# Kernel tuning notes

Hardware: AMD Instinct MI355X
Metric: run time of the kernel (lower is better)

The kernel has to match this reference:

```python
import jax, jax.numpy as jnp
import numpy as np
from jax import lax

R, BS, NATM, NORB = 2, 128, 81, 240
M_DIM = 16


def _init(key, shape, scale=0.05):
    return (jax.random.normal(key, shape) * scale).astype(jnp.float32)


def setup_inputs() -> dict:
    key = jax.random.key(0)
    ks = jax.random.split(key, 24)
    return {
        "xyz": jax.random.normal(ks[0], (R, BS, NATM, 3), jnp.float32) * 3.0,
        "cn": jax.random.uniform(ks[1], (R, BS, NATM), jnp.float32),
        "edisp": jax.random.normal(ks[2], (R, BS, NATM), jnp.float32),
        "ovlp": jax.random.normal(ks[3], (R, BS, NORB, NORB), jnp.float32),
        "h0": jax.random.normal(ks[4], (R, BS, NORB, NORB), jnp.float32),
        "egfn1": jax.random.normal(ks[5], (R, BS), jnp.float32),
        "nu": jax.random.normal(ks[6], (BS, R), jnp.float32),
        # EGNN(dim=2): edge_input_dim = 2*dim + 1 = 5
        "We1": _init(ks[7], (10, 5)), "be1": jnp.zeros((10,), jnp.float32),
        "We2": _init(ks[8], (M_DIM, 10)), "be2": jnp.zeros((M_DIM,), jnp.float32),
        "Wc1": _init(ks[9], (M_DIM * 4, M_DIM)), "bc1": jnp.zeros((M_DIM * 4,), jnp.float32),
        "Wc2": _init(ks[10], (1, M_DIM * 4)), "bc2": jnp.zeros((1,), jnp.float32),
        "coors_scale": jnp.full((1,), 1e-2, jnp.float32),
        "Wn1": _init(ks[11], (4, 2 + M_DIM)), "bn1": jnp.zeros((4,), jnp.float32),
        "Wn2": _init(ks[12], (2, 4)), "bn2": jnp.zeros((2,), jnp.float32),
        "conv1_w": _init(ks[13], (2, 1, 2, 2), 0.2), "conv1_b": jnp.zeros((2,), jnp.float32),
        "conv2_w": _init(ks[14], (2, 2, 2, 2), 0.2), "conv2_b": jnp.zeros((2,), jnp.float32),
        "fc1_w": _init(ks[15], (60, 14087), 0.01), "fc1_b": jnp.zeros((60,), jnp.float32),
        "fc2_w": _init(ks[16], (30, 60)), "fc2_b": jnp.zeros((30,), jnp.float32),
        "fc3_w": _init(ks[17], (1, 30)), "fc3_b": jnp.zeros((1,), jnp.float32),
    }


def _egnn(feats, coors, We1, be1, We2, be2, Wc1, bc1, Wc2, bc2, scale, Wn1, bn1, Wn2, bn2):
    # feats: (b, n, 2), coors: (b, n, 3); dense all-pairs EGNN layer (lucidrains defaults)
    b, n, d = feats.shape
    rel = coors[:, :, None, :] - coors[:, None, :, :]            # (b, i, j, 3)
    rel_dist = jnp.sum(rel * rel, axis=-1, keepdims=True)        # (b, i, j, 1) squared dist
    fi = jnp.broadcast_to(feats[:, :, None, :], (b, n, n, d))
    fj = jnp.broadcast_to(feats[:, None, :, :], (b, n, n, d))
    edge_in = jnp.concatenate([fi, fj, rel_dist], axis=-1)       # (b, i, j, 5)
    m = jax.nn.silu(edge_in @ We1.T + be1)
    m = jax.nn.silu(m @ We2.T + be2)                             # (b, i, j, M_DIM)
    cw = (jax.nn.silu(m @ Wc1.T + bc1) @ Wc2.T + bc2)[..., 0]    # (b, i, j)
    # CoorsNorm: unit-normalize rel coords, learned scale (init 1e-2)
    norm = jnp.sqrt(jnp.clip(rel_dist, 1e-16, None))
    rel_n = rel / norm * scale
    coors_out = jnp.einsum('bij,bijc->bic', cw, rel_n) + coors
    m_i = jnp.sum(m, axis=2)                                     # sum pooling over j
    node_in = jnp.concatenate([feats, m_i], axis=-1)
    feats_out = jax.nn.silu(node_in @ Wn1.T + bn1) @ Wn2.T + bn2 + feats
    return feats_out, coors_out


def _maxpool2(x):
    return lax.reduce_window(x, -jnp.inf, lax.max, (1, 1, 2, 2), (1, 1, 2, 2), 'VALID')


def _conv_block(x, w1, b1, w2, b2):
    # x: (b, N, N) -> NCHW conv stack matching conv1/pool/conv2/pool
    x = x[:, None, :, :]
    x = lax.conv_general_dilated(x, w1, (1, 1), 'VALID', dimension_numbers=('NCHW', 'OIHW', 'NCHW'))
    x = _maxpool2(jax.nn.leaky_relu(x + b1[None, :, None, None]))
    x = lax.conv_general_dilated(x, w2, (1, 1), 'VALID', dimension_numbers=('NCHW', 'OIHW', 'NCHW'))
    x = _maxpool2(jax.nn.leaky_relu(x + b2[None, :, None, None]))
    return x


def reference(xyz, cn, edisp, ovlp, h0, egfn1, nu,
              We1, be1, We2, be2, Wc1, bc1, Wc2, bc2, coors_scale,
              Wn1, bn1, Wn2, bn2, conv1_w, conv1_b, conv2_w, conv2_b,
              fc1_w, fc1_b, fc2_w, fc2_b, fc3_w, fc3_b):
    contribs = []
    for i in range(R):  # fixed small reactant list, mirrors the Python loop
        feats = jnp.stack([cn[i], edisp[i]], axis=-1)            # (bs, n_atms, 2)
        atm, _ = _egnn(feats, xyz[i], We1, be1, We2, be2, Wc1, bc1, Wc2, bc2,
                       coors_scale, Wn1, bn1, Wn2, bn2)
        o = _conv_block(ovlp[i], conv1_w, conv1_b, conv2_w, conv2_b)
        h = _conv_block(h0[i], conv1_w, conv1_b, conv2_w, conv2_b)
        x = jnp.concatenate([o, h], axis=1).reshape(o.shape[0], -1)   # (bs, 4*59*59)
        x = jnp.concatenate([x, atm.reshape(atm.shape[0], -1), egfn1[i][:, None]], axis=1)
        x = jax.nn.leaky_relu(x @ fc1_w.T + fc1_b)
        x = jax.nn.leaky_relu(x @ fc2_w.T + fc2_b)
        x = x @ fc3_w.T + fc3_b                                   # (bs, 1)
        contribs.append(x * nu[:, i][:, None])
    return jnp.sum(jnp.concatenate(contribs, axis=1), axis=1)    # (bs,)
```

## Files before the change

### kernel.cpp

```cpp
#include <hip/hip_runtime.h>
#include <hip/hip_bf16.h>

#define XDIM 14087
#define NATM 81
#define BS   128
#define KC   128
#define NKCH 111

__device__ __forceinline__ float fast_rcp(float x) {
    return __builtin_amdgcn_rcpf(x);
}
__device__ __forceinline__ float silu(float z) {
    return z * fast_rcp(1.f + __expf(-z));
}
__device__ __forceinline__ float leaky(float z) {
    return (z > 0.f) ? z : 0.01f * z;
}

__global__ __launch_bounds__(512) void egnn_kernel(
    const float* __restrict__ xyz, const float* __restrict__ cn,
    const float* __restrict__ edisp, const float* __restrict__ egfn1,
    const float* __restrict__ We1, const float* __restrict__ be1,
    const float* __restrict__ We2, const float* __restrict__ be2,
    const float* __restrict__ Wn1, const float* __restrict__ bn1,
    const float* __restrict__ Wn2, const float* __restrict__ bn2,
    float* __restrict__ xbuf)
{
    const int bid = blockIdx.x;
    const int tid = threadIdx.x;

    __shared__ float sc[NATM][3];
    __shared__ float sf[NATM][2];
    __shared__ float sai[NATM][10];
    __shared__ float sbj[NATM][10];
    __shared__ float sW2[160];
    __shared__ float sbe2[16];
    __shared__ float sw5[10];
    __shared__ float sWn1[72];
    __shared__ float sbn1[4];
    __shared__ float sWn2[8];
    __shared__ float sbn2[2];
    __shared__ float smp[3][NATM][17];

    const float* xb = xyz + (size_t)bid * NATM * 3;
    for (int idx = tid; idx < NATM * 3; idx += 512) sc[idx / 3][idx % 3] = xb[idx];
    if (tid < NATM) {
        const float f0 = cn[(size_t)bid * NATM + tid];
        const float f1 = edisp[(size_t)bid * NATM + tid];
        sf[tid][0] = f0; sf[tid][1] = f1;
        #pragma unroll
        for (int k = 0; k < 10; ++k) {
            sai[tid][k] = be1[k] + We1[k * 5 + 0] * f0 + We1[k * 5 + 1] * f1;
            sbj[tid][k] =          We1[k * 5 + 2] * f0 + We1[k * 5 + 3] * f1;
        }
    }
    if (tid < 160) sW2[tid] = We2[tid];
    if (tid < 16)  sbe2[tid] = be2[tid];
    if (tid < 10)  sw5[tid] = We1[tid * 5 + 4];
    if (tid < 72)  sWn1[tid] = Wn1[tid];
    if (tid < 4)   sbn1[tid] = bn1[tid];
    if (tid < 8)   sWn2[tid] = Wn2[tid];
    if (tid < 2)   sbn2[tid] = bn2[tid];
    __syncthreads();

    if (tid < 486) {
        const int i    = tid % 81;
        const int part = (tid / 81) % 3;
        const int half = tid / 243;

        float W2r[80];
        #pragma unroll
        for (int q = 0; q < 80; ++q) W2r[q] = sW2[half * 80 + q];
        float be2r[8];
        #pragma unroll
        for (int q = 0; q < 8; ++q) be2r[q] = sbe2[half * 8 + q];
        float w5r[10];
        #pragma unroll
        for (int k = 0; k < 10; ++k) w5r[k] = sw5[k];
        float air[10];
        #pragma unroll
        for (int k = 0; k < 10; ++k) air[k] = sai[i][k];
        const float ci0 = sc[i][0], ci1 = sc[i][1], ci2 = sc[i][2];

        float macc[8];
        #pragma unroll
        for (int q = 0; q < 8; ++q) macc[q] = 0.f;

        const int j0 = part * 27;
        for (int j = j0; j < j0 + 27; ++j) {
            const float dx = ci0 - sc[j][0];
            const float dy = ci1 - sc[j][1];
            const float dz = ci2 - sc[j][2];
            const float rd = dx * dx + dy * dy + dz * dz;
            float h[10];
            #pragma unroll
            for (int k = 0; k < 10; ++k) {
                const float z = air[k] + sbj[j][k] + w5r[k] * rd;
                h[k] = silu(z);
            }
            #pragma unroll
            for (int q = 0; q < 8; ++q) {
                float z = be2r[q];
                #pragma unroll
                for (int k = 0; k < 10; ++k) z += W2r[q * 10 + k] * h[k];
                macc[q] += silu(z);
            }
        }
        #pragma unroll
        for (int q = 0; q < 8; ++q) smp[part][i][half * 8 + q] = macc[q];
    }
    __syncthreads();

    if (tid < NATM) {
        float mi[16];
        #pragma unroll
        for (int q = 0; q < 16; ++q)
            mi[q] = smp[0][tid][q] + smp[1][tid][q] + smp[2][tid][q];
        const float f0 = sf[tid][0], f1 = sf[tid][1];
        float n1[4];
        #pragma unroll
        for (int k = 0; k < 4; ++k) {
            float z = sbn1[k] + sWn1[k * 18 + 0] * f0 + sWn1[k * 18 + 1] * f1;
            #pragma unroll
            for (int q = 0; q < 16; ++q) z += sWn1[k * 18 + 2 + q] * mi[q];
            n1[k] = silu(z);
        }
        float* xrow = xbuf + (size_t)bid * XDIM + 13924 + tid * 2;
        #pragma unroll
        for (int c = 0; c < 2; ++c) {
            float z = sbn2[c] + (c ? f1 : f0);
            #pragma unroll
            for (int k = 0; k < 4; ++k) z += sWn2[c * 4 + k] * n1[k];
            xrow[c] = z;
        }
    }
    if (tid == 0) xbuf[(size_t)bid * XDIM + 14086] = egfn1[bid];
}

__global__ __launch_bounds__(256) void conv_kernel(
    const float* __restrict__ ovlp, const float* __restrict__ h0,
    const float* __restrict__ w1, const float* __restrict__ b1,
    const float* __restrict__ w2, const float* __restrict__ b2,
    float* __restrict__ xbuf)
{
    const int bid   = blockIdx.x;
    const int strip = bid % 15;
    const int img   = bid / 15;
    const int b     = img & 127;
    const int t     = (img >> 7) & 1;
    const int r     = img >> 8;
    const int tid   = threadIdx.x;

    const int wv = tid >> 6;
    const int l  = tid & 63;
    const int y  = strip * 4 + wv;
    const int x  = l;
    if (x >= 59 || y >= 59) return;

    const float4* src4 = reinterpret_cast<const float4*>(
        (t ? h0 : ovlp) + (size_t)(r * BS + b) * 57600);

    float w1r[8], w2r[16], b1r[2], b2r[2];
    #pragma unroll
    for (int k = 0; k < 8; ++k) w1r[k] = w1[k];
    #pragma unroll
    for (int k = 0; k < 16; ++k) w2r[k] = w2[k];
    b1r[0] = b1[0]; b1r[1] = b1[1];
    b2r[0] = b2[0]; b2r[1] = b2[1];

    float P[7][8];
    const int base = 4 * y * 60 + x;
    #pragma unroll
    for (int rr = 0; rr < 7; ++rr) {
        const float4 a  = src4[base + rr * 60];
        const float4 bq = src4[base + rr * 60 + 1];
        P[rr][0] = a.x;  P[rr][1] = a.y;  P[rr][2] = a.z;  P[rr][3] = a.w;
        P[rr][4] = bq.x; P[rr][5] = bq.y; P[rr][6] = bq.z; P[rr][7] = bq.w;
    }

    float p1[2][3][3];
    #pragma unroll
    for (int c = 0; c < 2; ++c) {
        const float wa = w1r[c * 4 + 0], wb = w1r[c * 4 + 1];
        const float wc = w1r[c * 4 + 2], wd = w1r[c * 4 + 3];
        const float bb = b1r[c];
        #pragma unroll
        for (int pp = 0; pp < 3; ++pp)
        #pragma unroll
        for (int qq = 0; qq < 3; ++qq) {
            float mx = -3.4e38f;
            #pragma unroll
            for (int s = 0; s < 2; ++s)
            #pragma unroll
            for (int tt = 0; tt < 2; ++tt) {
                const int u = 2 * pp + s, v = 2 * qq + tt;
                float a = fmaf(wa, P[u][v], fmaf(wb, P[u][v + 1],
                          fmaf(wc, P[u + 1][v], fmaf(wd, P[u + 1][v + 1], bb))));
                a = leaky(a);
                mx = fmaxf(mx, a);
            }
            p1[c][pp][qq] = mx;
        }
    }

    float* xrow = xbuf + (size_t)(r * BS + b) * XDIM + (size_t)(t * 2) * 3481
                  + y * 59 + x;
    #pragma unroll
    for (int c2 = 0; c2 < 2; ++c2) {
        float mx = -3.4e38f;
        #pragma unroll
        for (int a2 = 0; a2 < 2; ++a2)
        #pragma unroll
        for (int b2i = 0; b2i < 2; ++b2i) {
            float acc = b2r[c2];
            #pragma unroll
            for (int c1 = 0; c1 < 2; ++c1)
            #pragma unroll
            for (int du = 0; du < 2; ++du)
            #pragma unroll
            for (int dv = 0; dv < 2; ++dv)
                acc += w2r[((c2 * 2 + c1) * 2 + du) * 2 + dv]
                     * p1[c1][a2 + du][b2i + dv];
            mx = fmaxf(mx, leaky(acc));
        }
        xrow[(size_t)c2 * 3481] = mx;
    }
}

__global__ __launch_bounds__(256) void gemm_fc1_kernel(
    const float* __restrict__ xbuf, const float* __restrict__ fc1w,
    float* __restrict__ psum)
{
    const int kc   = blockIdx.x;
    const int mt   = blockIdx.y;
    const int tid  = threadIdx.x;
    const int kbase = kc * KC;
    const int rem   = min(KC, XDIM - kbase);
    const int row0  = mt * 32;

    __shared__ float4 X4[32][33];
    __shared__ float4 W4[64][33];

    float* Xs = reinterpret_cast<float*>(&X4[0][0]);
    float* Ws = reinterpret_cast<float*>(&W4[0][0]);

    for (int idx = tid; idx < 32 * KC; idx += 256) {
        const int m = idx >> 7, k = idx & 127;
        Xs[m * 132 + k] = (k < rem) ? xbuf[(size_t)(row0 + m) * XDIM + kbase + k] : 0.f;
    }
    for (int idx = tid; idx < 64 * KC; idx += 256) {
        const int n = idx >> 7, k = idx & 127;
        Ws[n * 132 + k] = (n < 60 && k < rem) ? fc1w[(size_t)n * XDIM + kbase + k] : 0.f;
    }
    __syncthreads();

    const int ty = tid >> 4, tx = tid & 15;
    const int m0 = ty * 2;

    float acc[2][4];
    #pragma unroll
    for (int i = 0; i < 2; ++i)
    #pragma unroll
    for (int j = 0; j < 4; ++j) acc[i][j] = 0.f;

    #pragma unroll 4
    for (int k4 = 0; k4 < 32; ++k4) {
        const float4 xa = X4[m0][k4];
        const float4 xb = X4[m0 + 1][k4];
        #pragma unroll
        for (int j = 0; j < 4; ++j) {
            const float4 w = W4[tx + 16 * j][k4];
            acc[0][j] += xa.x * w.x + xa.y * w.y + xa.z * w.z + xa.w * w.w;
            acc[1][j] += xb.x * w.x + xb.y * w.y + xb.z * w.z + xb.w * w.w;
        }
    }

    float* po = psum + ((size_t)kc * 256 + row0) * 64;
    #pragma unroll
    for (int i = 0; i < 2; ++i)
    #pragma unroll
    for (int j = 0; j < 4; ++j)
        po[(size_t)(m0 + i) * 64 + tx + 16 * j] = acc[i][j];
}

__global__ __launch_bounds__(128) void fc_tail_kernel(
    const float* __restrict__ psum,
    const float* __restrict__ fc1b,
    const float* __restrict__ fc2w, const float* __restrict__ fc2b,
    const float* __restrict__ fc3w, const float* __restrict__ fc3b,
    const float* __restrict__ nu, float* __restrict__ out)
{
    const int b = blockIdx.x;
    const int tid = threadIdx.x;
    const int rh = tid >> 6;
    const int n  = tid & 63;

    __shared__ float y1s[2][64];
    __shared__ float y2s[2][30];

    const int row = rh * 128 + b;
    float s = 0.f;
    #pragma unroll 8
    for (int kcc = 0; kcc < NKCH; ++kcc)
        s += psum[((size_t)kcc * 256 + row) * 64 + n];
    y1s[rh][n] = (n < 60) ? leaky(s + fc1b[n]) : 0.f;
    __syncthreads();

    if (n < 30) {
        float a2 = fc2b[n];
        const float* wr = fc2w + n * 60;
        #pragma unroll
        for (int k = 0; k < 60; ++k) a2 += wr[k] * y1s[rh][k];
        y2s[rh][n] = leaky(a2);
    }
    __syncthreads();

    if (tid == 0) {
        float acc_out = 0.f;
        #pragma unroll
        for (int r = 0; r < 2; ++r) {
            float a3 = fc3b[0];
            #pragma unroll
            for (int k = 0; k < 30; ++k) a3 += fc3w[k] * y2s[r][k];
            acc_out += a3 * nu[b * 2 + r];
        }
        out[b] = acc_out;
    }
}

extern "C" void kernel_launch(void* const* d_in, const int* in_sizes, int n_in,
                              void* d_out, int out_size, void* d_ws, size_t ws_size,
                              hipStream_t stream)
{
    const float* xyz   = (const float*)d_in[0];
    const float* cn    = (const float*)d_in[1];
    const float* edisp = (const float*)d_in[2];
    const float* ovlp  = (const float*)d_in[3];
    const float* h0    = (const float*)d_in[4];
    const float* egfn1 = (const float*)d_in[5];
    const float* nu    = (const float*)d_in[6];
    const float* We1   = (const float*)d_in[7];
    const float* be1   = (const float*)d_in[8];
    const float* We2   = (const float*)d_in[9];
    const float* be2   = (const float*)d_in[10];
    const float* Wn1   = (const float*)d_in[16];
    const float* bn1   = (const float*)d_in[17];
    const float* Wn2   = (const float*)d_in[18];
    const float* bn2   = (const float*)d_in[19];
    const float* c1w   = (const float*)d_in[20];
    const float* c1b   = (const float*)d_in[21];
    const float* c2w   = (const float*)d_in[22];
    const float* c2b   = (const float*)d_in[23];
    const float* fc1w  = (const float*)d_in[24];
    const float* fc1b  = (const float*)d_in[25];
    const float* fc2w  = (const float*)d_in[26];
    const float* fc2b  = (const float*)d_in[27];
    const float* fc3w  = (const float*)d_in[28];
    const float* fc3b  = (const float*)d_in[29];

    float* xbuf = (float*)d_ws;
    float* psum = (float*)((char*)d_ws + 14425088);
    float* out  = (float*)d_out;

    hipLaunchKernelGGL(egnn_kernel, dim3(256), dim3(512), 0, stream,
                       xyz, cn, edisp, egfn1, We1, be1, We2, be2,
                       Wn1, bn1, Wn2, bn2, xbuf);
    hipLaunchKernelGGL(conv_kernel, dim3(2 * 2 * BS * 15), dim3(256), 0, stream,
                       ovlp, h0, c1w, c1b, c2w, c2b, xbuf);
    hipLaunchKernelGGL(gemm_fc1_kernel, dim3(NKCH, 8), dim3(256), 0, stream,
                       xbuf, fc1w, psum);
    hipLaunchKernelGGL(fc_tail_kernel, dim3(128), dim3(128), 0, stream,
                       psum, fc1b, fc2w, fc2b, fc3w, fc3b, nu, out);
}
```

Before: 274.6 us.

## Compute two conv outputs per thread to share overlapping input loads

Each conv thread now produces two adjacent output columns, loading a 7x12 input window instead of 7x8, so the overlapping pool windows are read and computed once for both outputs. The grid becomes 8 strips of 8 rows per image instead of 15 strips of 4, with clamped indices and guarded stores replacing the early return. Leaky ReLU is moved after the max (valid because it is monotonic), which cuts activation work. In exchange, more registers are used per thread and the padded lanes do redundant work.

Measured after the change: 284.8 us. 3.7% more time.

```diff
diff --git a/kernel.cpp b/kernel.cpp
--- a/kernel.cpp
+++ b/kernel.cpp
@@ -144,18 +144,18 @@
     float* __restrict__ xbuf)
 {
     const int bid   = blockIdx.x;
-    const int strip = bid % 15;
-    const int img   = bid / 15;
+    const int strip = bid & 7;
+    const int img   = bid >> 3;
     const int b     = img & 127;
     const int t     = (img >> 7) & 1;
     const int r     = img >> 8;
     const int tid   = threadIdx.x;
 
-    const int wv = tid >> 6;
-    const int l  = tid & 63;
-    const int y  = strip * 4 + wv;
-    const int x  = l;
-    if (x >= 59 || y >= 59) return;
+    const int q    = tid & 31;
+    const int slot = tid >> 5;
+    const int y    = strip * 8 + slot;
+    const int qc   = (q < 30) ? q : 29;
+    const int yc   = (y < 59) ? y : 58;
 
     const float4* src4 = reinterpret_cast<const float4*>(
         (t ? h0 : ovlp) + (size_t)(r * BS + b) * 57600);
@@ -168,62 +168,70 @@
     b1r[0] = b1[0]; b1r[1] = b1[1];
     b2r[0] = b2[0]; b2r[1] = b2[1];
 
-    float P[7][8];
-    const int base = 4 * y * 60 + x;
+    float P[7][12];
+    const int rbase = 4 * yc * 60 + 2 * qc;
     #pragma unroll
     for (int rr = 0; rr < 7; ++rr) {
-        const float4 a  = src4[base + rr * 60];
-        const float4 bq = src4[base + rr * 60 + 1];
-        P[rr][0] = a.x;  P[rr][1] = a.y;  P[rr][2] = a.z;  P[rr][3] = a.w;
-        P[rr][4] = bq.x; P[rr][5] = bq.y; P[rr][6] = bq.z; P[rr][7] = bq.w;
-    }
-
-    float p1[2][3][3];
+        #pragma unroll
+        for (int c4 = 0; c4 < 3; ++c4) {
+            const int ci = 2 * qc + c4;
+            const float4 v = src4[4 * yc * 60 + rr * 60 + ((ci < 60) ? ci : 59)];
+            P[rr][c4 * 4 + 0] = v.x; P[rr][c4 * 4 + 1] = v.y;
+            P[rr][c4 * 4 + 2] = v.z; P[rr][c4 * 4 + 3] = v.w;
+        }
+    }
+
+    float p1[2][3][5];
     #pragma unroll
     for (int c = 0; c < 2; ++c) {
         const float wa = w1r[c * 4 + 0], wb = w1r[c * 4 + 1];
         const float wc = w1r[c * 4 + 2], wd = w1r[c * 4 + 3];
         const float bb = b1r[c];
         #pragma unroll
-        for (int pp = 0; pp < 3; ++pp)
-        #pragma unroll
-        for (int qq = 0; qq < 3; ++qq) {
+        for (int pr = 0; pr < 3; ++pr)
+        #pragma unroll
+        for (int pc = 0; pc < 5; ++pc) {
             float mx = -3.4e38f;
             #pragma unroll
             for (int s = 0; s < 2; ++s)
             #pragma unroll
             for (int tt = 0; tt < 2; ++tt) {
-                const int u = 2 * pp + s, v = 2 * qq + tt;
-                float a = fmaf(wa, P[u][v], fmaf(wb, P[u][v + 1],
-                          fmaf(wc, P[u + 1][v], fmaf(wd, P[u + 1][v + 1], bb))));
-                a = leaky(a);
-                mx = fmaxf(mx, a);
+                const int u = 2 * pr + s, v = 2 * pc + tt;
+                const float raw = fmaf(wa, P[u][v], fmaf(wb, P[u][v + 1],
+                                  fmaf(wc, P[u + 1][v], fmaf(wd, P[u + 1][v + 1], bb))));
+                mx = fmaxf(mx, raw);
             }
-            p1[c][pp][qq] = mx;
-        }
-    }
-
+            p1[c][pr][pc] = leaky(mx);
+        }
+    }
+
+    const bool wy = (y < 59) && (q < 30);
     float* xrow = xbuf + (size_t)(r * BS + b) * XDIM + (size_t)(t * 2) * 3481
-                  + y * 59 + x;
+                  + y * 59 + 2 * q;
     #pragma unroll
     for (int c2 = 0; c2 < 2; ++c2) {
-        float mx = -3.4e38f;
-        #pragma unroll
-        for (int a2 = 0; a2 < 2; ++a2)
-        #pragma unroll
-        for (int b2i = 0; b2i < 2; ++b2i) {
-            float acc = b2r[c2];
-            #pragma unroll
-            for (int c1 = 0; c1 < 2; ++c1)
-            #pragma unroll
-            for (int du = 0; du < 2; ++du)
-            #pragma unroll
-            for (int dv = 0; dv < 2; ++dv)
-                acc += w2r[((c2 * 2 + c1) * 2 + du) * 2 + dv]
-                     * p1[c1][a2 + du][b2i + dv];
-            mx = fmaxf(mx, leaky(acc));
-        }
-        xrow[(size_t)c2 * 3481] = mx;
+        #pragma unroll
+        for (int fx = 0; fx < 2; ++fx) {
+            float mx = -3.4e38f;
+            #pragma unroll
+            for (int a2 = 0; a2 < 2; ++a2)
+            #pragma unroll
+            for (int b2i = 0; b2i < 2; ++b2i) {
+                const int cc = 2 * fx + b2i;
+                float acc = b2r[c2];
+                #pragma unroll
+                for (int c1 = 0; c1 < 2; ++c1)
+                #pragma unroll
+                for (int du = 0; du < 2; ++du)
+                #pragma unroll
+                for (int dv = 0; dv < 2; ++dv)
+                    acc += w2r[((c2 * 2 + c1) * 2 + du) * 2 + dv]
+                         * p1[c1][a2 + du][cc + dv];
+                mx = fmaxf(mx, acc);
+            }
+            if (wy && (2 * q + fx < 59))
+                xrow[(size_t)c2 * 3481 + fx] = leaky(mx);
+        }
     }
 }
 
@@ -365,7 +373,7 @@
     hipLaunchKernelGGL(egnn_kernel, dim3(256), dim3(512), 0, stream,
                        xyz, cn, edisp, egfn1, We1, be1, We2, be2,
                        Wn1, bn1, Wn2, bn2, xbuf);
-    hipLaunchKernelGGL(conv_kernel, dim3(2 * 2 * BS * 15), dim3(256), 0, stream,
+    hipLaunchKernelGGL(conv_kernel, dim3(512 * 8), dim3(256), 0, stream,
                        ovlp, h0, c1w, c1b, c2w, c2b, xbuf);
     hipLaunchKernelGGL(gemm_fc1_kernel, dim3(NKCH, 8), dim3(256), 0, stream,
                        xbuf, fc1w, psum);
```

## Share conv1 pooled outputs across lanes via shuffles and split fc tail reduction

Applied to the files above, without the earlier changes.

In the conv kernel each lane now loads only 5 values per row instead of 8 and computes 2 of the 3 pooled conv1 columns. The third column comes from the neighbouring lane through a shuffle, which removes redundant loads and FMAs. Leaky ReLU is applied after the max-pool rather than before it, which is valid because leaky ReLU is monotonic. The fc tail kernel now splits the 111-chunk partial-sum reduction across 4 thread groups per row with a shared-memory combine, using 512 threads per block so the serial loop is shorter.

After: 272.4 us. Within noise of the previous version (-0.8%).

```diff
diff --git a/kernel.cpp b/kernel.cpp
--- a/kernel.cpp
+++ b/kernel.cpp
@@ -154,11 +154,11 @@
     const int wv = tid >> 6;
     const int l  = tid & 63;
     const int y  = strip * 4 + wv;
+    if (y >= 59) return;
     const int x  = l;
-    if (x >= 59 || y >= 59) return;
-
-    const float4* src4 = reinterpret_cast<const float4*>(
-        (t ? h0 : ovlp) + (size_t)(r * BS + b) * 57600);
+    const int xc = (x < 59) ? x : 59;
+
+    const float* src = (t ? h0 : ovlp) + (size_t)(r * BS + b) * 57600;
 
     float w1r[8], w2r[16], b1r[2], b2r[2];
     #pragma unroll
@@ -168,62 +168,72 @@
     b1r[0] = b1[0]; b1r[1] = b1[1];
     b2r[0] = b2[0]; b2r[1] = b2[1];
 
-    float P[7][8];
-    const int base = 4 * y * 60 + x;
+    float P[7][5];
     #pragma unroll
     for (int rr = 0; rr < 7; ++rr) {
-        const float4 a  = src4[base + rr * 60];
-        const float4 bq = src4[base + rr * 60 + 1];
-        P[rr][0] = a.x;  P[rr][1] = a.y;  P[rr][2] = a.z;  P[rr][3] = a.w;
-        P[rr][4] = bq.x; P[rr][5] = bq.y; P[rr][6] = bq.z; P[rr][7] = bq.w;
-    }
-
-    float p1[2][3][3];
+        const float* rp = src + (4 * y + rr) * 240 + 4 * xc;
+        const float4 a = *reinterpret_cast<const float4*>(rp);
+        P[rr][0] = a.x; P[rr][1] = a.y; P[rr][2] = a.z; P[rr][3] = a.w;
+        P[rr][4] = rp[4];
+    }
+
+    float p1o[2][3][2];
     #pragma unroll
     for (int c = 0; c < 2; ++c) {
         const float wa = w1r[c * 4 + 0], wb = w1r[c * 4 + 1];
         const float wc = w1r[c * 4 + 2], wd = w1r[c * 4 + 3];
         const float bb = b1r[c];
         #pragma unroll
-        for (int pp = 0; pp < 3; ++pp)
-        #pragma unroll
-        for (int qq = 0; qq < 3; ++qq) {
+        for (int pr = 0; pr < 3; ++pr)
+        #pragma unroll
+        for (int pc = 0; pc < 2; ++pc) {
             float mx = -3.4e38f;
             #pragma unroll
             for (int s = 0; s < 2; ++s)
             #pragma unroll
             for (int tt = 0; tt < 2; ++tt) {
-                const int u = 2 * pp + s, v = 2 * qq + tt;
-                float a = fmaf(wa, P[u][v], fmaf(wb, P[u][v + 1],
-                          fmaf(wc, P[u + 1][v], fmaf(wd, P[u + 1][v + 1], bb))));
-                a = leaky(a);
-                mx = fmaxf(mx, a);
+                const int u = 2 * pr + s, v = 2 * pc + tt;
+                const float raw = fmaf(wa, P[u][v], fmaf(wb, P[u][v + 1],
+                                  fmaf(wc, P[u + 1][v], fmaf(wd, P[u + 1][v + 1], bb))));
+                mx = fmaxf(mx, raw);
             }
-            p1[c][pp][qq] = mx;
-        }
-    }
-
-    float* xrow = xbuf + (size_t)(r * BS + b) * XDIM + (size_t)(t * 2) * 3481
-                  + y * 59 + x;
-    #pragma unroll
-    for (int c2 = 0; c2 < 2; ++c2) {
-        float mx = -3.4e38f;
-        #pragma unroll
-        for (int a2 = 0; a2 < 2; ++a2)
-        #pragma unroll
-        for (int b2i = 0; b2i < 2; ++b2i) {
-            float acc = b2r[c2];
-            #pragma unroll
-            for (int c1 = 0; c1 < 2; ++c1)
-            #pragma unroll
-            for (int du = 0; du < 2; ++du)
-            #pragma unroll
-            for (int dv = 0; dv < 2; ++dv)
-                acc += w2r[((c2 * 2 + c1) * 2 + du) * 2 + dv]
-                     * p1[c1][a2 + du][b2i + dv];
-            mx = fmaxf(mx, leaky(acc));
-        }
-        xrow[(size_t)c2 * 3481] = mx;
+            p1o[c][pr][pc] = leaky(mx);
+        }
+    }
+
+    float p1[2][3][3];
+    #pragma unroll
+    for (int c = 0; c < 2; ++c)
+    #pragma unroll
+    for (int pr = 0; pr < 3; ++pr) {
+        p1[c][pr][0] = p1o[c][pr][0];
+        p1[c][pr][1] = p1o[c][pr][1];
+        p1[c][pr][2] = __shfl_down(p1o[c][pr][0], 1);
+    }
+
+    if (x < 59) {
+        float* xrow = xbuf + (size_t)(r * BS + b) * XDIM + (size_t)(t * 2) * 3481
+                      + y * 59 + x;
+        #pragma unroll
+        for (int c2 = 0; c2 < 2; ++c2) {
+            float mx = -3.4e38f;
+            #pragma unroll
+            for (int a2 = 0; a2 < 2; ++a2)
+            #pragma unroll
+            for (int b2i = 0; b2i < 2; ++b2i) {
+                float acc = b2r[c2];
+                #pragma unroll
+                for (int c1 = 0; c1 < 2; ++c1)
+                #pragma unroll
+                for (int du = 0; du < 2; ++du)
+                #pragma unroll
+                for (int dv = 0; dv < 2; ++dv)
+                    acc += w2r[((c2 * 2 + c1) * 2 + du) * 2 + dv]
+                         * p1[c1][a2 + du][b2i + dv];
+                mx = fmaxf(mx, acc);
+            }
+            xrow[(size_t)c2 * 3481] = leaky(mx);
+        }
     }
 }
 
@@ -283,7 +293,7 @@
         po[(size_t)(m0 + i) * 64 + tx + 16 * j] = acc[i][j];
 }
 
-__global__ __launch_bounds__(128) void fc_tail_kernel(
+__global__ __launch_bounds__(512) void fc_tail_kernel(
     const float* __restrict__ psum,
     const float* __restrict__ fc1b,
     const float* __restrict__ fc2w, const float* __restrict__ fc2b,
@@ -292,21 +302,28 @@
 {
     const int b = blockIdx.x;
     const int tid = threadIdx.x;
-    const int rh = tid >> 6;
     const int n  = tid & 63;
-
+    const int kq = (tid >> 6) & 3;
+    const int rh = tid >> 8;
+
+    __shared__ float red[2][4][64];
     __shared__ float y1s[2][64];
     __shared__ float y2s[2][30];
 
     const int row = rh * 128 + b;
     float s = 0.f;
-    #pragma unroll 8
-    for (int kcc = 0; kcc < NKCH; ++kcc)
+    for (int kcc = kq; kcc < NKCH; kcc += 4)
         s += psum[((size_t)kcc * 256 + row) * 64 + n];
-    y1s[rh][n] = (n < 60) ? leaky(s + fc1b[n]) : 0.f;
-    __syncthreads();
-
-    if (n < 30) {
+    red[rh][kq][n] = s;
+    __syncthreads();
+
+    if (kq == 0) {
+        float t = red[rh][0][n] + red[rh][1][n] + red[rh][2][n] + red[rh][3][n];
+        y1s[rh][n] = (n < 60) ? leaky(t + fc1b[n]) : 0.f;
+    }
+    __syncthreads();
+
+    if (kq == 0 && n < 30) {
         float a2 = fc2b[n];
         const float* wr = fc2w + n * 60;
         #pragma unroll
@@ -369,6 +386,6 @@
                        ovlp, h0, c1w, c1b, c2w, c2b, xbuf);
     hipLaunchKernelGGL(gemm_fc1_kernel, dim3(NKCH, 8), dim3(256), 0, stream,
                        xbuf, fc1w, psum);
-    hipLaunchKernelGGL(fc_tail_kernel, dim3(128), dim3(128), 0, stream,
+    hipLaunchKernelGGL(fc_tail_kernel, dim3(128), dim3(512), 0, stream,
                        psum, fc1b, fc2w, fc2b, fc3w, fc3b, nu, out);
 }
```
